# Kernel optimization log

Measured on AMD Instinct MI355X. Metric: run time of the kernel, lower is better.

## Reference

```python
import jax, jax.numpy as jnp
import numpy as np


def setup_inputs() -> dict:
    key = jax.random.key(0)
    k1, k2, k3, k4 = jax.random.split(key, 4)
    B, T, N, C_IN, C_OUT, K = 32, 24, 1024, 64, 64, 3
    x = jax.random.normal(k1, (B, T, N, C_IN), dtype=jnp.float32)
    Tks = jax.random.normal(k2, (K, N, N), dtype=jnp.float32)
    # kaiming-uniform-ish init scale for Theta, small uniform bias
    bound_t = float(np.sqrt(6.0 / C_IN))
    Theta = jax.random.uniform(k3, (K, C_IN, C_OUT), dtype=jnp.float32,
                               minval=-bound_t, maxval=bound_t)
    bound_b = 1.0 / float(np.sqrt(C_IN))
    bias = jax.random.uniform(k4, (K, C_OUT), dtype=jnp.float32,
                              minval=-bound_b, maxval=bound_b)
    return {"x": x, "Tks": Tks, "Theta": Theta, "bias": bias}


def reference(x, Tks, Theta, bias):
    # torch.einsum('nn,btnc->btnc', T_k, x) extracts diag(T_k) and scales x per node.
    d = jnp.diagonal(Tks, axis1=1, axis2=2)  # [K, N]
    # sum_k diag(T_k) * x @ Theta_k  -> [B, T, N, C_OUT]
    out = jnp.einsum('kn,btnc,kco->btno', d, x, Theta)
    # each bias[k] is added once -> total additive term is sum over k
    out = out + jnp.sum(bias, axis=0)
    return out
```

## Files before the change

kernel.cpp:

```cpp
#include <hip/hip_runtime.h>


#define NNODES 1024
#define TILE_ROWS 64
#define NT 8
#define ROWS_PER_BLOCK (TILE_ROWS * NT)
#define NBLOCKS (786432 / ROWS_PER_BLOCK)

#define WS_W  0
#define WS_BS (24 * 1024)
#define WS_DV (24 * 1024 + 256)

typedef __attribute__((ext_vector_type(8))) short short8;
typedef __attribute__((ext_vector_type(4))) float f32x4;
typedef __attribute__((ext_vector_type(4))) int   i32x4;

__device__ __forceinline__ unsigned short f2bf(float f) {
    union { float f; unsigned u; } v; v.f = f;
    unsigned r = v.u + 0x7FFFu + ((v.u >> 16) & 1u);
    return (unsigned short)(r >> 16);
}

__device__ __forceinline__ int cvt_pk_bf16(float lo, float hi) {
    int r;
    asm("v_cvt_pk_bf16_f32 %0, %1, %2" : "=v"(r) : "v"(lo), "v"(hi));
    return r;
}

__device__ __forceinline__ void gload_lds16(const void* g, void* l) {
    __builtin_amdgcn_global_load_lds(
        (const __attribute__((address_space(1))) void*)g,
        (__attribute__((address_space(3))) void*)l,
        16, 0, 0);
}

__global__ void cheb_prep(const float* __restrict__ Tks,
                          const float* __restrict__ Theta,
                          const float* __restrict__ bias,
                          unsigned char* __restrict__ ws) {
    const int b = blockIdx.x;
    const int l = threadIdx.x;
    if (b < 24) {
        const int kc = b >> 3, h = (b >> 2) & 1, nb = b & 3;
        const int o  = nb * 16 + (l & 15);
        const int cb = h * 32 + (l >> 4) * 8;
        unsigned short* dst = (unsigned short*)(ws + WS_W) + ((size_t)b * 64 + l) * 8;
        #pragma unroll
        for (int j = 0; j < 8; ++j)
            dst[j] = f2bf(Theta[kc * 4096 + (cb + j) * 64 + o]);
    } else if (b < 40) {
        const int n = (b - 24) * 64 + l;
        const size_t dg = (size_t)n * (NNODES + 1);
        f32x4 v;
        v[0] = Tks[dg];
        v[1] = Tks[(size_t)NNODES * NNODES + dg];
        v[2] = Tks[(size_t)2 * NNODES * NNODES + dg];
        v[3] = 0.0f;
        *((f32x4*)(ws + WS_DV) + n) = v;
    } else {
        float* bs = (float*)(ws + WS_BS);
        bs[l] = bias[l] + bias[64 + l] + bias[128 + l];
    }
}

__global__ __launch_bounds__(512, 4) void cheb_main(
    const float* __restrict__ x,
    const unsigned char* __restrict__ ws,
    float* __restrict__ out)
{
    __shared__ float xs[3][TILE_ROWS * 64];
    __shared__ __align__(16) float dvs[ROWS_PER_BLOCK][4];

    const int tid  = threadIdx.x;
    const int wave = tid >> 6;
    const int lane = tid & 63;
    const int lrow = lane & 15;
    const int lgrp = lane >> 4;
    const int wr   = wave >> 1;
    const int q    = wave & 1;
    const size_t rowbase = (size_t)blockIdx.x * ROWS_PER_BLOCK;

    const unsigned short* wimg = (const unsigned short*)(ws + WS_W);
    const float*          bsum = (const float*)(ws + WS_BS);
    const f32x4*          dvec = (const f32x4*)(ws + WS_DV);

    short8 wf[3][2][2];
    #pragma unroll
    for (int kc = 0; kc < 3; ++kc)
        #pragma unroll
        for (int h = 0; h < 2; ++h)
            #pragma unroll
            for (int nb = 0; nb < 2; ++nb)
                wf[kc][h][nb] = *(const short8*)(
                    wimg + ((size_t)(((kc * 2 + h) * 4 + q * 2 + nb) * 64 + lane)) * 8);

    f32x4 bs4[2];
    #pragma unroll
    for (int nb = 0; nb < 2; ++nb)
        bs4[nb] = *(const f32x4*)(bsum + q * 32 + nb * 16 + lgrp * 4);

    gload_lds16((const char*)dvec + (((rowbase + wave * 64) & (NNODES - 1)) * 16 + lane * 16),
                &dvs[wave * 64][0]);

#define STAGE(T) do { if ((T) < NT) {                                         \
        _Pragma("unroll")                                                     \
        for (int s = 0; s < 2; ++s) {                                         \
            const int u_ = wave * 2 + s;                                      \
            const int R_ = u_ * 4 + lgrp;                                     \
            const int c_ = (lrow * 16) ^ ((R_ & 7) << 4);                     \
            const char* g_ = (const char*)x +                                 \
                (((rowbase + (size_t)(T) * TILE_ROWS + R_) << 8) + c_);       \
            gload_lds16(g_, (char*)&xs[(T) % 3][0] + u_ * 1024);              \
        } } } while (0)

#define WAITV(N) do {                                                         \
        asm volatile("s_waitcnt vmcnt(" #N ")" ::: "memory");                 \
        __builtin_amdgcn_sched_barrier(0);                                    \
        __builtin_amdgcn_s_barrier();                                         \
        __builtin_amdgcn_sched_barrier(0);                                    \
    } while (0)

#define BODY(T) do {                                                          \
        const int R = wr * 16 + lrow;                                         \
        const int m_ = (lrow & 7) << 4;                                       \
        const char* rowp = (const char*)&xs[(T) % 3][0] + R * 256;            \
        const int c00 = (lgrp * 32) ^ m_;                                     \
        const int c01 = (lgrp * 32 + 16) ^ m_;                                \
        const f32x4 x0 = *(const f32x4*)(rowp + c00);                         \
        const f32x4 x1 = *(const f32x4*)(rowp + c01);                         \
        const f32x4 x2 = *(const f32x4*)(rowp + 128 + c00);                   \
        const f32x4 x3 = *(const f32x4*)(rowp + 128 + c01);                   \
        const f32x4 dv = *(const f32x4*)(&dvs[(T) * TILE_ROWS + R][0]);       \
        short8 xf[3][2];                                                      \
        _Pragma("unroll")                                                     \
        for (int kc = 0; kc < 3; ++kc) {                                      \
            const float dk = dv[kc];                                          \
            i32x4 r0, r1;                                                     \
            r0[0] = cvt_pk_bf16(dk * x0[0], dk * x0[1]);                      \
            r0[1] = cvt_pk_bf16(dk * x0[2], dk * x0[3]);                      \
            r0[2] = cvt_pk_bf16(dk * x1[0], dk * x1[1]);                      \
            r0[3] = cvt_pk_bf16(dk * x1[2], dk * x1[3]);                      \
            r1[0] = cvt_pk_bf16(dk * x2[0], dk * x2[1]);                      \
            r1[1] = cvt_pk_bf16(dk * x2[2], dk * x2[3]);                      \
            r1[2] = cvt_pk_bf16(dk * x3[0], dk * x3[1]);                      \
            r1[3] = cvt_pk_bf16(dk * x3[2], dk * x3[3]);                      \
            xf[kc][0] = __builtin_bit_cast(short8, r0);                       \
            xf[kc][1] = __builtin_bit_cast(short8, r1);                       \
        }                                                                     \
        f32x4 acc[2] = {f32x4{0,0,0,0}, f32x4{0,0,0,0}};                      \
        _Pragma("unroll")                                                     \
        for (int kc = 0; kc < 3; ++kc)                                        \
            _Pragma("unroll")                                                 \
            for (int h = 0; h < 2; ++h)                                       \
                _Pragma("unroll")                                             \
                for (int nb = 0; nb < 2; ++nb)                                \
                    acc[nb] = __builtin_amdgcn_mfma_f32_16x16x32_bf16(        \
                        wf[kc][h][nb], xf[kc][h], acc[nb], 0, 0, 0);          \
        float* orow = out + (rowbase + (size_t)(T) * TILE_ROWS + R) * 64      \
                          + q * 32;                                           \
        _Pragma("unroll")                                                     \
        for (int nb = 0; nb < 2; ++nb) {                                      \
            f32x4 o4;                                                         \
            _Pragma("unroll")                                                 \
            for (int j = 0; j < 4; ++j) o4[j] = acc[nb][j] + bs4[nb][j];      \
            *(f32x4*)(orow + nb * 16 + lgrp * 4) = o4;                        \
        }                                                                     \
    } while (0)

    STAGE(0); STAGE(1);
    WAITV(2); STAGE(2);  BODY(0);
    WAITV(4); STAGE(3);  BODY(1);
    WAITV(6); STAGE(4);  BODY(2);
    WAITV(6); STAGE(5);  BODY(3);
    WAITV(6); STAGE(6);  BODY(4);
    WAITV(6); STAGE(7);  BODY(5);
    WAITV(6); STAGE(8);  BODY(6);
    WAITV(4); STAGE(9);  BODY(7);

#undef STAGE
#undef WAITV
#undef BODY
}

extern "C" void kernel_launch(void* const* d_in, const int* in_sizes, int n_in,
                              void* d_out, int out_size, void* d_ws, size_t ws_size,
                              hipStream_t stream) {
    const float* x     = (const float*)d_in[0];
    const float* Tks   = (const float*)d_in[1];
    const float* Theta = (const float*)d_in[2];
    const float* bias  = (const float*)d_in[3];
    float* out = (float*)d_out;
    unsigned char* ws = (unsigned char*)d_ws;

    hipLaunchKernelGGL(cheb_prep, dim3(41), dim3(64), 0, stream,
                       Tks, Theta, bias, ws);
    hipLaunchKernelGGL(cheb_main, dim3(NBLOCKS), dim3(512), 0, stream,
                       x, ws, out);
}
```

Baseline: 90.30 us.

## Replace LDS-staged x tiles with direct register prefetch in smaller blocks

Drops the triple-buffered LDS staging of x, along with the per-tile barriers. Each lane now loads its x fragments straight from global memory into registers, with a three-deep rotating register prefetch controlled by explicit vmcnt waits. Block size goes from 512 to 256 threads and tiles shrink to 32 rows, so each block covers 256 rows and more blocks are launched. The aim is to remove LDS traffic and barrier stalls in this bandwidth-bound kernel. The cost is that both waves of a pair load the same x rows, and the vmcnt waits are conservative and may stall more than needed.

```diff
diff --git a/kernel.cpp b/kernel.cpp
--- a/kernel.cpp
+++ b/kernel.cpp
@@ -2,9 +2,8 @@
 
 
 #define NNODES 1024
-#define TILE_ROWS 64
 #define NT 8
-#define ROWS_PER_BLOCK (TILE_ROWS * NT)
+#define ROWS_PER_BLOCK 256
 #define NBLOCKS (786432 / ROWS_PER_BLOCK)
 
 #define WS_W  0
@@ -63,12 +62,11 @@
     }
 }
 
-__global__ __launch_bounds__(512, 4) void cheb_main(
+__global__ __launch_bounds__(256, 3) void cheb_main(
     const float* __restrict__ x,
     const unsigned char* __restrict__ ws,
     float* __restrict__ out)
 {
-    __shared__ float xs[3][TILE_ROWS * 64];
     __shared__ __align__(16) float dvs[ROWS_PER_BLOCK][4];
 
     const int tid  = threadIdx.x;
@@ -78,11 +76,12 @@
     const int lgrp = lane >> 4;
     const int wr   = wave >> 1;
     const int q    = wave & 1;
+    const int R    = wr * 16 + lrow;
     const size_t rowbase = (size_t)blockIdx.x * ROWS_PER_BLOCK;
 
     const unsigned short* wimg = (const unsigned short*)(ws + WS_W);
     const float*          bsum = (const float*)(ws + WS_BS);
-    const f32x4*          dvec = (const f32x4*)(ws + WS_DV);
+    const float*          dvec = (const float*)(ws + WS_DV);
 
     short8 wf[3][2][2];
     #pragma unroll
@@ -99,54 +98,39 @@
     for (int nb = 0; nb < 2; ++nb)
         bs4[nb] = *(const f32x4*)(bsum + q * 32 + nb * 16 + lgrp * 4);
 
-    gload_lds16((const char*)dvec + (((rowbase + wave * 64) & (NNODES - 1)) * 16 + lane * 16),
+    gload_lds16((const char*)dvec + ((rowbase + wave * 64) & (NNODES - 1)) * 16 + lane * 16,
                 &dvs[wave * 64][0]);
+    __syncthreads();
 
-#define STAGE(T) do { if ((T) < NT) {                                         \
-        _Pragma("unroll")                                                     \
-        for (int s = 0; s < 2; ++s) {                                         \
-            const int u_ = wave * 2 + s;                                      \
-            const int R_ = u_ * 4 + lgrp;                                     \
-            const int c_ = (lrow * 16) ^ ((R_ & 7) << 4);                     \
-            const char* g_ = (const char*)x +                                 \
-                (((rowbase + (size_t)(T) * TILE_ROWS + R_) << 8) + c_);       \
-            gload_lds16(g_, (char*)&xs[(T) % 3][0] + u_ * 1024);              \
-        } } } while (0)
+#define LOADX(T, X0, X1, X2, X3) do { if ((T) < NT) {                         \
+        const float* xr_ = x + (rowbase + (T) * 32 + R) * 64;                 \
+        X0 = *(const f32x4*)(xr_ + lgrp * 8);                                 \
+        X1 = *(const f32x4*)(xr_ + lgrp * 8 + 4);                             \
+        X2 = *(const f32x4*)(xr_ + 32 + lgrp * 8);                            \
+        X3 = *(const f32x4*)(xr_ + 32 + lgrp * 8 + 4);                        \
+    } } while (0)
 
-#define WAITV(N) do {                                                         \
+#define ITER(T, N, X0, X1, X2, X3) do {                                       \
+        const f32x4 dv = *(const f32x4*)(&dvs[(T) * 32 + R][0]);              \
         asm volatile("s_waitcnt vmcnt(" #N ")" ::: "memory");                 \
         __builtin_amdgcn_sched_barrier(0);                                    \
-        __builtin_amdgcn_s_barrier();                                         \
-        __builtin_amdgcn_sched_barrier(0);                                    \
-    } while (0)
-
-#define BODY(T) do {                                                          \
-        const int R = wr * 16 + lrow;                                         \
-        const int m_ = (lrow & 7) << 4;                                       \
-        const char* rowp = (const char*)&xs[(T) % 3][0] + R * 256;            \
-        const int c00 = (lgrp * 32) ^ m_;                                     \
-        const int c01 = (lgrp * 32 + 16) ^ m_;                                \
-        const f32x4 x0 = *(const f32x4*)(rowp + c00);                         \
-        const f32x4 x1 = *(const f32x4*)(rowp + c01);                         \
-        const f32x4 x2 = *(const f32x4*)(rowp + 128 + c00);                   \
-        const f32x4 x3 = *(const f32x4*)(rowp + 128 + c01);                   \
-        const f32x4 dv = *(const f32x4*)(&dvs[(T) * TILE_ROWS + R][0]);       \
         short8 xf[3][2];                                                      \
         _Pragma("unroll")                                                     \
         for (int kc = 0; kc < 3; ++kc) {                                      \
             const float dk = dv[kc];                                          \
             i32x4 r0, r1;                                                     \
-            r0[0] = cvt_pk_bf16(dk * x0[0], dk * x0[1]);                      \
-            r0[1] = cvt_pk_bf16(dk * x0[2], dk * x0[3]);                      \
-            r0[2] = cvt_pk_bf16(dk * x1[0], dk * x1[1]);                      \
-            r0[3] = cvt_pk_bf16(dk * x1[2], dk * x1[3]);                      \
-            r1[0] = cvt_pk_bf16(dk * x2[0], dk * x2[1]);                      \
-            r1[1] = cvt_pk_bf16(dk * x2[2], dk * x2[3]);                      \
-            r1[2] = cvt_pk_bf16(dk * x3[0], dk * x3[1]);                      \
-            r1[3] = cvt_pk_bf16(dk * x3[2], dk * x3[3]);                      \
+            r0[0] = cvt_pk_bf16(dk * X0[0], dk * X0[1]);                      \
+            r0[1] = cvt_pk_bf16(dk * X0[2], dk * X0[3]);                      \
+            r0[2] = cvt_pk_bf16(dk * X1[0], dk * X1[1]);                      \
+            r0[3] = cvt_pk_bf16(dk * X1[2], dk * X1[3]);                      \
+            r1[0] = cvt_pk_bf16(dk * X2[0], dk * X2[1]);                      \
+            r1[1] = cvt_pk_bf16(dk * X2[2], dk * X2[3]);                      \
+            r1[2] = cvt_pk_bf16(dk * X3[0], dk * X3[1]);                      \
+            r1[3] = cvt_pk_bf16(dk * X3[2], dk * X3[3]);                      \
             xf[kc][0] = __builtin_bit_cast(short8, r0);                       \
             xf[kc][1] = __builtin_bit_cast(short8, r1);                       \
         }                                                                     \
+        LOADX((T) + 3, X0, X1, X2, X3);          \
         f32x4 acc[2] = {f32x4{0,0,0,0}, f32x4{0,0,0,0}};                      \
         _Pragma("unroll")                                                     \
         for (int kc = 0; kc < 3; ++kc)                                        \
@@ -156,8 +140,7 @@
                 for (int nb = 0; nb < 2; ++nb)                                \
                     acc[nb] = __builtin_amdgcn_mfma_f32_16x16x32_bf16(        \
                         wf[kc][h][nb], xf[kc][h], acc[nb], 0, 0, 0);          \
-        float* orow = out + (rowbase + (size_t)(T) * TILE_ROWS + R) * 64      \
-                          + q * 32;                                           \
+        float* orow = out + (rowbase + (T) * 32 + R) * 64 + q * 32;           \
         _Pragma("unroll")                                                     \
         for (int nb = 0; nb < 2; ++nb) {                                      \
             f32x4 o4;                                                         \
@@ -167,19 +150,21 @@
         }                                                                     \
     } while (0)
 
-    STAGE(0); STAGE(1);
-    WAITV(2); STAGE(2);  BODY(0);
-    WAITV(4); STAGE(3);  BODY(1);
-    WAITV(6); STAGE(4);  BODY(2);
-    WAITV(6); STAGE(5);  BODY(3);
-    WAITV(6); STAGE(6);  BODY(4);
-    WAITV(6); STAGE(7);  BODY(5);
-    WAITV(6); STAGE(8);  BODY(6);
-    WAITV(4); STAGE(9);  BODY(7);
+    f32x4 a0, a1, a2, a3, b0, b1, b2, b3, c0, c1, c2, c3;
+    LOADX(0, a0, a1, a2, a3);
+    LOADX(1, b0, b1, b2, b3);
+    LOADX(2, c0, c1, c2, c3);
+    ITER(0, 4,  a0, a1, a2, a3);
+    ITER(1, 6,  b0, b1, b2, b3);
+    ITER(2, 8,  c0, c1, c2, c3);
+    ITER(3, 10, a0, a1, a2, a3);
+    ITER(4, 10, b0, b1, b2, b3);
+    ITER(5, 10, c0, c1, c2, c3);
+    ITER(6, 6,  a0, a1, a2, a3);
+    ITER(7, 2,  b0, b1, b2, b3);
 
-#undef STAGE
-#undef WAITV
-#undef BODY
+#undef LOADX
+#undef ITER
 }
 
 extern "C" void kernel_launch(void* const* d_in, const int* in_sizes, int n_in,
@@ -194,6 +179,6 @@
 
     hipLaunchKernelGGL(cheb_prep, dim3(41), dim3(64), 0, stream,
                        Tks, Theta, bias, ws);
-    hipLaunchKernelGGL(cheb_main, dim3(NBLOCKS), dim3(512), 0, stream,
+    hipLaunchKernelGGL(cheb_main, dim3(NBLOCKS), dim3(256), 0, stream,
                        x, ws, out);
 }
```

Measured after the change: 105.2 us. 1.17x slower.

## Stage outputs through LDS for coalesced nontemporal stores, keep diag scales in registers

Applied to the files above, without the earlier changes.

MFMA results are now written to a double-buffered, swizzled LDS output tile. In the next pipeline step each row is stored to global memory as full contiguous 256-byte rows with nontemporal stores, replacing the scattered 16-byte fragment stores. The per-node diagonal scales are preloaded into registers instead of being staged through LDS. MFMA sections are wrapped in s_setprio, and the wait counts are adjusted because the new stores add vmcnt entries. This adds LDS traffic, an extra barrier and more register use, and the changed vmcnt accounting must stay correct.

```diff
diff --git a/kernel.cpp b/kernel.cpp
--- a/kernel.cpp
+++ b/kernel.cpp
@@ -69,7 +69,7 @@
     float* __restrict__ out)
 {
     __shared__ float xs[3][TILE_ROWS * 64];
-    __shared__ __align__(16) float dvs[ROWS_PER_BLOCK][4];
+    __shared__ float outb[2][4][16 * 64];
 
     const int tid  = threadIdx.x;
     const int wave = tid >> 6;
@@ -80,9 +80,9 @@
     const int q    = wave & 1;
     const size_t rowbase = (size_t)blockIdx.x * ROWS_PER_BLOCK;
 
-    const unsigned short* wimg = (const unsigned short*)(ws + WS_W);
-    const float*          bsum = (const float*)(ws + WS_BS);
-    const f32x4*          dvec = (const f32x4*)(ws + WS_DV);
+    const unsigned short* wimg  = (const unsigned short*)(ws + WS_W);
+    const float*          bsum  = (const float*)(ws + WS_BS);
+    const f32x4*          dvec4 = (const f32x4*)(ws + WS_DV);
 
     short8 wf[3][2][2];
     #pragma unroll
@@ -99,8 +99,12 @@
     for (int nb = 0; nb < 2; ++nb)
         bs4[nb] = *(const f32x4*)(bsum + q * 32 + nb * 16 + lgrp * 4);
 
-    gload_lds16((const char*)dvec + (((rowbase + wave * 64) & (NNODES - 1)) * 16 + lane * 16),
-                &dvs[wave * 64][0]);
+    float d0[NT], d1[NT], d2[NT];
+    #pragma unroll
+    for (int t = 0; t < NT; ++t) {
+        const f32x4 dv = dvec4[(rowbase + t * TILE_ROWS + wr * 16 + lrow) & (NNODES - 1)];
+        d0[t] = dv[0]; d1[t] = dv[1]; d2[t] = dv[2];
+    }
 
 #define STAGE(T) do { if ((T) < NT) {                                         \
         _Pragma("unroll")                                                     \
@@ -113,28 +117,40 @@
             gload_lds16(g_, (char*)&xs[(T) % 3][0] + u_ * 1024);              \
         } } } while (0)
 
-#define WAITV(N) do {                                                         \
-        asm volatile("s_waitcnt vmcnt(" #N ")" ::: "memory");                 \
+#define WAITB(N) do {                                                         \
+        asm volatile("s_waitcnt vmcnt(" #N ") lgkmcnt(0)" ::: "memory");      \
         __builtin_amdgcn_sched_barrier(0);                                    \
         __builtin_amdgcn_s_barrier();                                         \
         __builtin_amdgcn_sched_barrier(0);                                    \
     } while (0)
 
+#define EPILOG(T) do { if ((T) >= 0) {                                        \
+        _Pragma("unroll")                                                     \
+        for (int r = 0; r < 2; ++r) {                                         \
+            const int rl = q * 8 + r * 4 + lgrp;                              \
+            const int byt = (lrow * 16) ^ ((rl & 7) << 4);                    \
+            const f32x4 v = *(const f32x4*)(                                  \
+                (const char*)&outb[(T) & 1][wr][0] + rl * 256 + byt);         \
+            __builtin_nontemporal_store(v, (f32x4*)((char*)(out +             \
+                (rowbase + (size_t)(T) * TILE_ROWS + wr * 16 + rl) * 64)      \
+                + lrow * 16));                                                \
+        } } } while (0)
+
 #define BODY(T) do {                                                          \
-        const int R = wr * 16 + lrow;                                         \
         const int m_ = (lrow & 7) << 4;                                       \
-        const char* rowp = (const char*)&xs[(T) % 3][0] + R * 256;            \
+        const char* rowp = (const char*)&xs[(T) % 3][0]                       \
+                         + (wr * 16 + lrow) * 256;                            \
         const int c00 = (lgrp * 32) ^ m_;                                     \
         const int c01 = (lgrp * 32 + 16) ^ m_;                                \
         const f32x4 x0 = *(const f32x4*)(rowp + c00);                         \
         const f32x4 x1 = *(const f32x4*)(rowp + c01);                         \
         const f32x4 x2 = *(const f32x4*)(rowp + 128 + c00);                   \
         const f32x4 x3 = *(const f32x4*)(rowp + 128 + c01);                   \
-        const f32x4 dv = *(const f32x4*)(&dvs[(T) * TILE_ROWS + R][0]);       \
+        const float dk0 = d0[T], dk1 = d1[T], dk2 = d2[T];                    \
         short8 xf[3][2];                                                      \
         _Pragma("unroll")                                                     \
         for (int kc = 0; kc < 3; ++kc) {                                      \
-            const float dk = dv[kc];                                          \
+            const float dk = kc == 0 ? dk0 : (kc == 1 ? dk1 : dk2);           \
             i32x4 r0, r1;                                                     \
             r0[0] = cvt_pk_bf16(dk * x0[0], dk * x0[1]);                      \
             r0[1] = cvt_pk_bf16(dk * x0[2], dk * x0[3]);                      \
@@ -148,6 +164,7 @@
             xf[kc][1] = __builtin_bit_cast(short8, r1);                       \
         }                                                                     \
         f32x4 acc[2] = {f32x4{0,0,0,0}, f32x4{0,0,0,0}};                      \
+        __builtin_amdgcn_s_setprio(1);                                        \
         _Pragma("unroll")                                                     \
         for (int kc = 0; kc < 3; ++kc)                                        \
             _Pragma("unroll")                                                 \
@@ -156,29 +173,33 @@
                 for (int nb = 0; nb < 2; ++nb)                                \
                     acc[nb] = __builtin_amdgcn_mfma_f32_16x16x32_bf16(        \
                         wf[kc][h][nb], xf[kc][h], acc[nb], 0, 0, 0);          \
-        float* orow = out + (rowbase + (size_t)(T) * TILE_ROWS + R) * 64      \
-                          + q * 32;                                           \
+        __builtin_amdgcn_s_setprio(0);                                        \
         _Pragma("unroll")                                                     \
         for (int nb = 0; nb < 2; ++nb) {                                      \
             f32x4 o4;                                                         \
             _Pragma("unroll")                                                 \
             for (int j = 0; j < 4; ++j) o4[j] = acc[nb][j] + bs4[nb][j];      \
-            *(f32x4*)(orow + nb * 16 + lgrp * 4) = o4;                        \
+            const int byt = (q * 128 + nb * 64 + lgrp * 16) ^ m_;             \
+            *(f32x4*)((char*)&outb[(T) & 1][wr][0] + lrow * 256 + byt) = o4;  \
         }                                                                     \
     } while (0)
 
     STAGE(0); STAGE(1);
-    WAITV(2); STAGE(2);  BODY(0);
-    WAITV(4); STAGE(3);  BODY(1);
-    WAITV(6); STAGE(4);  BODY(2);
-    WAITV(6); STAGE(5);  BODY(3);
-    WAITV(6); STAGE(6);  BODY(4);
-    WAITV(6); STAGE(7);  BODY(5);
-    WAITV(6); STAGE(8);  BODY(6);
-    WAITV(4); STAGE(9);  BODY(7);
+    WAITB(0); STAGE(2);  EPILOG(-1); BODY(0);
+    WAITB(0); STAGE(3);  EPILOG(0);  BODY(1);
+    WAITB(2); STAGE(4);  EPILOG(1);  BODY(2);
+    WAITB(4); STAGE(5);  EPILOG(2);  BODY(3);
+    WAITB(4); STAGE(6);  EPILOG(3);  BODY(4);
+    WAITB(4); STAGE(7);  EPILOG(4);  BODY(5);
+    WAITB(4); STAGE(8);  EPILOG(5);  BODY(6);
+    WAITB(2); STAGE(9);  EPILOG(6);  BODY(7);
+    asm volatile("s_waitcnt lgkmcnt(0)" ::: "memory");
+    __builtin_amdgcn_s_barrier();
+    EPILOG(7);
 
 #undef STAGE
-#undef WAITV
+#undef WAITB
+#undef EPILOG
 #undef BODY
 }
 
```

After: 122.4 us. 35.6% more time.
